# Optimization experiments

Hardware: AMD Instinct MI355X
Metric: run time of the kernel (lower is better)

The kernel has to match this reference:

```python
import jax, jax.numpy as jnp
import numpy as np

S = 14
C = 20
STEP = 1.0 / 14
LAMBDA_COORD = 3.0
LAMBDA_NOOBJ = 0.3
LAMBDA_OBJ = 1.0
LAMBDA_CLS = 1.5


def setup_inputs() -> dict:
    key = jax.random.key(0)
    k1, k2 = jax.random.split(key)
    batch = 4096
    pred = jax.random.normal(k1, (batch, S, S, 30), dtype=jnp.float32)
    target = jax.random.normal(k2, (batch, S, S, 30), dtype=jnp.float32)
    return {"pred": pred, "target": target}


def _convert_boxes(box):
    # box: [B, S, S, 2, 4] in (cx, cy, w, h) grid-relative coords
    # grid index i is the x (third) axis, j the y (second) axis, per forward's [x, y]
    gi = jnp.arange(S, dtype=box.dtype)[None, None, :, None]  # x index
    gj = jnp.arange(S, dtype=box.dtype)[None, :, None, None]  # y index
    x = (box[..., 0] + gi) * STEP - box[..., 2] * 0.5
    y = (box[..., 1] + gj) * STEP - box[..., 3] * 0.5
    out = jnp.stack([x, y, box[..., 2], box[..., 3]], axis=-1)
    return jnp.maximum(out, 0.0)  # torch.clamp(box, min=0) on the whole box


def _iou(b1, b2):
    x1, y1, w1, h1 = b1[..., 0], b1[..., 1], b1[..., 2], b1[..., 3]
    x2, y2, w2, h2 = b2[..., 0], b2[..., 1], b2[..., 2], b2[..., 3]
    inter_w = jnp.maximum(w1 + w2 - (jnp.maximum(x1 + w1, x2 + w2) - jnp.minimum(x1, x2)), 0.0)
    inter_h = jnp.maximum(h1 + h2 - (jnp.maximum(y1 + h1, y2 + h2) - jnp.minimum(y1, y2)), 0.0)
    inter = inter_w * inter_h
    union = w1 * h1 + w2 * h2 - inter
    return inter / (union + 1e-6)


def _smooth_l1_sum(p, t, mask):
    d = p - t
    ad = jnp.abs(d)
    l = jnp.where(ad < 1.0, 0.5 * d * d, ad - 0.5)
    return jnp.sum(l * mask)


def reference(pred, target):
    batch = pred.shape[0]
    pb = pred[..., :10].reshape(batch, S, S, 2, 5)
    tb = target[..., :10].reshape(batch, S, S, 2, 5)
    pred_cls = pred[..., 10:]
    target_cls = target[..., 10:]

    obj_mask = tb[..., 4] > 0          # [B,S,S,2]
    sig_mask = obj_mask[..., 1]         # [B,S,S]

    # responsible-box selection: elementwise IoU between pred box k and target box k
    ious = _iou(_convert_boxes(pb[..., :4]), _convert_boxes(tb[..., :4]))  # [B,S,S,2]
    max_i = jnp.argmax(ious, axis=-1)   # first-max, matches torch .max(0)
    keep = jnp.arange(2) == max_i[..., None]
    obj_mask = jnp.where(sig_mask[..., None], obj_mask & keep, obj_mask)
    noobj_mask = ~obj_mask

    om = obj_mask.astype(pred.dtype)
    nm = noobj_mask.astype(pred.dtype)

    conf_sq = (pb[..., 4] - tb[..., 4]) ** 2
    noobj_loss = jnp.sum(conf_sq * nm)
    obj_loss = jnp.sum(conf_sq * om)

    xy_loss = _smooth_l1_sum(pb[..., :2], tb[..., :2], om[..., None])
    wh_loss = _smooth_l1_sum(
        jnp.sqrt(jnp.maximum(pb[..., 2:4], 1e-6)),
        jnp.sqrt(jnp.maximum(tb[..., 2:4], 1e-6)),
        om[..., None],
    )

    logp = jax.nn.log_softmax(pred_cls, axis=-1)
    tgt_idx = jnp.argmax(target_cls, axis=-1)  # [B,S,S]
    nll = -jnp.take_along_axis(logp, tgt_idx[..., None], axis=-1)[..., 0]
    class_loss = jnp.sum(nll * sig_mask.astype(pred.dtype))

    total = (LAMBDA_COORD * (xy_loss + wh_loss)
             + LAMBDA_OBJ * obj_loss
             + LAMBDA_NOOBJ * noobj_loss
             + LAMBDA_CLS * class_loss) / batch
    return total
```

## Files before the change

### kernel.cpp

```cpp
#include <hip/hip_runtime.h>
#include <math.h>

#define SS 14
#define NCLS 20
#define CELL_FLOATS 30
#define BLOCK 256
#define CPB 128
#define FPB (CPB * CELL_FLOATS)
#define F4PB (FPB / 4)

__device__ __forceinline__ float smooth_l1(float d) {
    float ad = fabsf(d);
    return ad < 1.0f ? 0.5f * d * d : ad - 0.5f;
}

__device__ __forceinline__ void conv_box(const float* b, float gi, float gj,
                                         float& x, float& y, float& w, float& h) {
    const float STEP = 1.0f / 14.0f;
    x = fmaxf((b[0] + gi) * STEP - b[2] * 0.5f, 0.0f);
    y = fmaxf((b[1] + gj) * STEP - b[3] * 0.5f, 0.0f);
    w = fmaxf(b[2], 0.0f);
    h = fmaxf(b[3], 0.0f);
}

__device__ __forceinline__ float iou_box(float x1, float y1, float w1, float h1,
                                         float x2, float y2, float w2, float h2) {
    float iw = fmaxf(w1 + w2 - (fmaxf(x1 + w1, x2 + w2) - fminf(x1, x2)), 0.0f);
    float ih = fmaxf(h1 + h2 - (fmaxf(y1 + h1, y2 + h2) - fminf(y1, y2)), 0.0f);
    float inter = iw * ih;
    float uni = w1 * h1 + w2 * h2 - inter;
    return inter / (uni + 1e-6f);
}

__global__ __launch_bounds__(BLOCK) void yolo_loss_kernel(
    const float4* __restrict__ pred4, const float4* __restrict__ target4,
    float* __restrict__ partials, int ncells, float inv_batch) {
    __shared__ float sp[FPB];
    __shared__ float st[FPB];

    const int tid = threadIdx.x;
    const long long total4 = ((long long)ncells * CELL_FLOATS) / 4;
    const long long base4 = (long long)blockIdx.x * F4PB;

#pragma unroll
    for (int k = 0; k < 4; ++k) {
        int i = tid + k * BLOCK;
        if (i < F4PB && base4 + i < total4) {
            ((float4*)sp)[i] = pred4[base4 + i];
            ((float4*)st)[i] = target4[base4 + i];
        }
    }
    __syncthreads();

    int cell = blockIdx.x * CPB + tid;
    float tot = 0.0f;
    if (tid < CPB && cell < ncells) {
        float p[CELL_FLOATS], t[CELL_FLOATS];
        const float2* pp = (const float2*)(sp + tid * CELL_FLOATS);
        const float2* tp = (const float2*)(st + tid * CELL_FLOATS);
#pragma unroll
        for (int k = 0; k < CELL_FLOATS / 2; ++k) {
            ((float2*)p)[k] = pp[k];
            ((float2*)t)[k] = tp[k];
        }

        int rc = cell % (SS * SS);
        float gj = (float)(rc / SS);
        float gi = (float)(rc % SS);

        float px, py, pw, ph, tx, ty, tw, th;
        conv_box(p + 0, gi, gj, px, py, pw, ph);
        conv_box(t + 0, gi, gj, tx, ty, tw, th);
        float iou0 = iou_box(px, py, pw, ph, tx, ty, tw, th);
        conv_box(p + 5, gi, gj, px, py, pw, ph);
        conv_box(t + 5, gi, gj, tx, ty, tw, th);
        float iou1 = iou_box(px, py, pw, ph, tx, ty, tw, th);

        bool obj0 = t[4] > 0.0f;
        bool obj1 = t[9] > 0.0f;
        bool sig = obj1;
        bool m1 = iou1 > iou0;
        bool om0 = sig ? (obj0 && !m1) : obj0;
        bool om1 = sig ? m1 : false;

        float c0 = p[4] - t[4]; c0 *= c0;
        float c1 = p[9] - t[9]; c1 *= c1;
        float obj_l = (om0 ? c0 : 0.0f) + (om1 ? c1 : 0.0f);
        float noobj_l = (om0 ? 0.0f : c0) + (om1 ? 0.0f : c1);

        float xy = 0.0f, wh = 0.0f;
        if (om0) {
            xy += smooth_l1(p[0] - t[0]) + smooth_l1(p[1] - t[1]);
            wh += smooth_l1(sqrtf(fmaxf(p[2], 1e-6f)) - sqrtf(fmaxf(t[2], 1e-6f)));
            wh += smooth_l1(sqrtf(fmaxf(p[3], 1e-6f)) - sqrtf(fmaxf(t[3], 1e-6f)));
        }
        if (om1) {
            xy += smooth_l1(p[5] - t[5]) + smooth_l1(p[6] - t[6]);
            wh += smooth_l1(sqrtf(fmaxf(p[7], 1e-6f)) - sqrtf(fmaxf(t[7], 1e-6f)));
            wh += smooth_l1(sqrtf(fmaxf(p[8], 1e-6f)) - sqrtf(fmaxf(t[8], 1e-6f)));
        }

        float cls = 0.0f;
        {
            float m = p[10];
#pragma unroll
            for (int c = 1; c < NCLS; ++c) m = fmaxf(m, p[10 + c]);
            float se = 0.0f;
#pragma unroll
            for (int c = 0; c < NCLS; ++c) se += expf(p[10 + c] - m);
            float bt = t[10];
            int bi = 0;
#pragma unroll
            for (int c = 1; c < NCLS; ++c) {
                if (t[10 + c] > bt) { bt = t[10 + c]; bi = c; }
            }
            float logp = p[10 + bi] - m - logf(se);
            cls = sig ? -logp : 0.0f;
        }

        tot = 3.0f * (xy + wh) + obj_l + 0.3f * noobj_l + 1.5f * cls;
        tot *= inv_batch;
    }

#pragma unroll
    for (int off = 32; off > 0; off >>= 1) tot += __shfl_down(tot, off, 64);
    __shared__ float wsum[4];
    int lane = threadIdx.x & 63;
    int wid = threadIdx.x >> 6;
    if (lane == 0) wsum[wid] = tot;
    __syncthreads();
    if (threadIdx.x == 0) {
        partials[blockIdx.x] = wsum[0] + wsum[1] + wsum[2] + wsum[3];
    }
}

__global__ __launch_bounds__(BLOCK) void reduce_kernel(
    const float* __restrict__ partials, float* __restrict__ out, int n) {
    float s = 0.0f;
    for (int i = threadIdx.x; i < n; i += BLOCK) s += partials[i];
#pragma unroll
    for (int off = 32; off > 0; off >>= 1) s += __shfl_down(s, off, 64);
    __shared__ float wsum[4];
    int lane = threadIdx.x & 63;
    int wid = threadIdx.x >> 6;
    if (lane == 0) wsum[wid] = s;
    __syncthreads();
    if (threadIdx.x == 0) out[0] = wsum[0] + wsum[1] + wsum[2] + wsum[3];
}

extern "C" void kernel_launch(void* const* d_in, const int* in_sizes, int n_in,
                              void* d_out, int out_size, void* d_ws, size_t ws_size,
                              hipStream_t stream) {
    const float4* pred4 = (const float4*)d_in[0];
    const float4* target4 = (const float4*)d_in[1];
    float* out = (float*)d_out;
    float* partials = (float*)d_ws;

    int total = in_sizes[0];
    int ncells = total / CELL_FLOATS;
    int batch = ncells / (SS * SS);
    float inv_batch = 1.0f / (float)batch;

    int grid = (ncells + CPB - 1) / CPB;
    yolo_loss_kernel<<<grid, BLOCK, 0, stream>>>(pred4, target4, partials, ncells, inv_batch);
    reduce_kernel<<<1, BLOCK, 0, stream>>>(partials, out, grid);
}
```

Before: 230.9 us.

## Process four tiles per block with register-prefetched double buffering

Each block now handles four 128-cell tiles in sequence. The next tile's global loads go into registers while the current tile is computed from shared memory. This overlaps memory latency with compute and cuts the grid size and the partials count by four. It also switches expf/logf to the fast __expf/__logf intrinsics, which slightly lowers precision. Fewer blocks could reduce parallelism, and the extra syncs add some cost.

```diff
diff --git a/kernel.cpp b/kernel.cpp
--- a/kernel.cpp
+++ b/kernel.cpp
@@ -5,9 +5,10 @@
 #define NCLS 20
 #define CELL_FLOATS 30
 #define BLOCK 256
-#define CPB 128
-#define FPB (CPB * CELL_FLOATS)
-#define F4PB (FPB / 4)
+#define TILE 128
+#define TPB_TILES 4
+#define FPT (TILE * CELL_FLOATS)
+#define F4PT (FPT / 4)
 
 __device__ __forceinline__ float smooth_l1(float d) {
     float ad = fabsf(d);
@@ -32,102 +33,140 @@
     return inter / (uni + 1e-6f);
 }
 
+__device__ __forceinline__ float cell_loss(const float* __restrict__ p,
+                                           const float* __restrict__ t, int cell) {
+    int rc = cell % (SS * SS);
+    float gj = (float)(rc / SS);
+    float gi = (float)(rc % SS);
+
+    float px, py, pw, ph, tx, ty, tw, th;
+    conv_box(p + 0, gi, gj, px, py, pw, ph);
+    conv_box(t + 0, gi, gj, tx, ty, tw, th);
+    float iou0 = iou_box(px, py, pw, ph, tx, ty, tw, th);
+    conv_box(p + 5, gi, gj, px, py, pw, ph);
+    conv_box(t + 5, gi, gj, tx, ty, tw, th);
+    float iou1 = iou_box(px, py, pw, ph, tx, ty, tw, th);
+
+    bool obj0 = t[4] > 0.0f;
+    bool obj1 = t[9] > 0.0f;
+    bool sig = obj1;
+    bool m1 = iou1 > iou0;
+    bool om0 = sig ? (obj0 && !m1) : obj0;
+    bool om1 = sig ? m1 : false;
+
+    float c0 = p[4] - t[4]; c0 *= c0;
+    float c1 = p[9] - t[9]; c1 *= c1;
+    float obj_l = (om0 ? c0 : 0.0f) + (om1 ? c1 : 0.0f);
+    float noobj_l = (om0 ? 0.0f : c0) + (om1 ? 0.0f : c1);
+
+    float xy = 0.0f, wh = 0.0f;
+    if (om0) {
+        xy += smooth_l1(p[0] - t[0]) + smooth_l1(p[1] - t[1]);
+        wh += smooth_l1(sqrtf(fmaxf(p[2], 1e-6f)) - sqrtf(fmaxf(t[2], 1e-6f)));
+        wh += smooth_l1(sqrtf(fmaxf(p[3], 1e-6f)) - sqrtf(fmaxf(t[3], 1e-6f)));
+    }
+    if (om1) {
+        xy += smooth_l1(p[5] - t[5]) + smooth_l1(p[6] - t[6]);
+        wh += smooth_l1(sqrtf(fmaxf(p[7], 1e-6f)) - sqrtf(fmaxf(t[7], 1e-6f)));
+        wh += smooth_l1(sqrtf(fmaxf(p[8], 1e-6f)) - sqrtf(fmaxf(t[8], 1e-6f)));
+    }
+
+    float cls = 0.0f;
+    {
+        float m = p[10];
+#pragma unroll
+        for (int c = 1; c < NCLS; ++c) m = fmaxf(m, p[10 + c]);
+        float se = 0.0f;
+#pragma unroll
+        for (int c = 0; c < NCLS; ++c) se += __expf(p[10 + c] - m);
+        float bt = t[10];
+        int bi = 0;
+#pragma unroll
+        for (int c = 1; c < NCLS; ++c) {
+            if (t[10 + c] > bt) { bt = t[10 + c]; bi = c; }
+        }
+        float logp = p[10 + bi] - m - __logf(se);
+        cls = sig ? -logp : 0.0f;
+    }
+
+    return 3.0f * (xy + wh) + obj_l + 0.3f * noobj_l + 1.5f * cls;
+}
+
 __global__ __launch_bounds__(BLOCK) void yolo_loss_kernel(
     const float4* __restrict__ pred4, const float4* __restrict__ target4,
-    float* __restrict__ partials, int ncells, float inv_batch) {
-    __shared__ float sp[FPB];
-    __shared__ float st[FPB];
+    float* __restrict__ partials, int ncells, int ntiles, float inv_batch) {
+    __shared__ float sp[FPT];
+    __shared__ float st[FPT];
 
     const int tid = threadIdx.x;
+    const int tile0 = blockIdx.x * TPB_TILES;
     const long long total4 = ((long long)ncells * CELL_FLOATS) / 4;
-    const long long base4 = (long long)blockIdx.x * F4PB;
-
-#pragma unroll
-    for (int k = 0; k < 4; ++k) {
-        int i = tid + k * BLOCK;
-        if (i < F4PB && base4 + i < total4) {
-            ((float4*)sp)[i] = pred4[base4 + i];
-            ((float4*)st)[i] = target4[base4 + i];
-        }
-    }
-    __syncthreads();
-
-    int cell = blockIdx.x * CPB + tid;
-    float tot = 0.0f;
-    if (tid < CPB && cell < ncells) {
-        float p[CELL_FLOATS], t[CELL_FLOATS];
-        const float2* pp = (const float2*)(sp + tid * CELL_FLOATS);
-        const float2* tp = (const float2*)(st + tid * CELL_FLOATS);
-#pragma unroll
-        for (int k = 0; k < CELL_FLOATS / 2; ++k) {
-            ((float2*)p)[k] = pp[k];
-            ((float2*)t)[k] = tp[k];
-        }
-
-        int rc = cell % (SS * SS);
-        float gj = (float)(rc / SS);
-        float gi = (float)(rc % SS);
-
-        float px, py, pw, ph, tx, ty, tw, th;
-        conv_box(p + 0, gi, gj, px, py, pw, ph);
-        conv_box(t + 0, gi, gj, tx, ty, tw, th);
-        float iou0 = iou_box(px, py, pw, ph, tx, ty, tw, th);
-        conv_box(p + 5, gi, gj, px, py, pw, ph);
-        conv_box(t + 5, gi, gj, tx, ty, tw, th);
-        float iou1 = iou_box(px, py, pw, ph, tx, ty, tw, th);
-
-        bool obj0 = t[4] > 0.0f;
-        bool obj1 = t[9] > 0.0f;
-        bool sig = obj1;
-        bool m1 = iou1 > iou0;
-        bool om0 = sig ? (obj0 && !m1) : obj0;
-        bool om1 = sig ? m1 : false;
-
-        float c0 = p[4] - t[4]; c0 *= c0;
-        float c1 = p[9] - t[9]; c1 *= c1;
-        float obj_l = (om0 ? c0 : 0.0f) + (om1 ? c1 : 0.0f);
-        float noobj_l = (om0 ? 0.0f : c0) + (om1 ? 0.0f : c1);
-
-        float xy = 0.0f, wh = 0.0f;
-        if (om0) {
-            xy += smooth_l1(p[0] - t[0]) + smooth_l1(p[1] - t[1]);
-            wh += smooth_l1(sqrtf(fmaxf(p[2], 1e-6f)) - sqrtf(fmaxf(t[2], 1e-6f)));
-            wh += smooth_l1(sqrtf(fmaxf(p[3], 1e-6f)) - sqrtf(fmaxf(t[3], 1e-6f)));
-        }
-        if (om1) {
-            xy += smooth_l1(p[5] - t[5]) + smooth_l1(p[6] - t[6]);
-            wh += smooth_l1(sqrtf(fmaxf(p[7], 1e-6f)) - sqrtf(fmaxf(t[7], 1e-6f)));
-            wh += smooth_l1(sqrtf(fmaxf(p[8], 1e-6f)) - sqrtf(fmaxf(t[8], 1e-6f)));
-        }
-
-        float cls = 0.0f;
-        {
-            float m = p[10];
-#pragma unroll
-            for (int c = 1; c < NCLS; ++c) m = fmaxf(m, p[10 + c]);
-            float se = 0.0f;
-#pragma unroll
-            for (int c = 0; c < NCLS; ++c) se += expf(p[10 + c] - m);
-            float bt = t[10];
-            int bi = 0;
-#pragma unroll
-            for (int c = 1; c < NCLS; ++c) {
-                if (t[10 + c] > bt) { bt = t[10 + c]; bi = c; }
-            }
-            float logp = p[10 + bi] - m - logf(se);
-            cls = sig ? -logp : 0.0f;
-        }
-
-        tot = 3.0f * (xy + wh) + obj_l + 0.3f * noobj_l + 1.5f * cls;
-        tot *= inv_batch;
-    }
-
-#pragma unroll
-    for (int off = 32; off > 0; off >>= 1) tot += __shfl_down(tot, off, 64);
+
+    float4 rp[4], rt[4];
+    float acc = 0.0f;
+
+    {
+        long long base4 = (long long)tile0 * F4PT;
+#pragma unroll
+        for (int k = 0; k < 4; ++k) {
+            int i = tid + k * BLOCK;
+            if (i < F4PT && base4 + i < total4) {
+                rp[k] = pred4[base4 + i];
+                rt[k] = target4[base4 + i];
+            }
+        }
+    }
+
+    for (int j = 0; j < TPB_TILES; ++j) {
+        int tt = tile0 + j;
+        if (tt >= ntiles) break;
+
+#pragma unroll
+        for (int k = 0; k < 4; ++k) {
+            int i = tid + k * BLOCK;
+            if (i < F4PT) {
+                ((float4*)sp)[i] = rp[k];
+                ((float4*)st)[i] = rt[k];
+            }
+        }
+        __syncthreads();
+
+        if (j + 1 < TPB_TILES && tt + 1 < ntiles) {
+            long long base4 = (long long)(tt + 1) * F4PT;
+#pragma unroll
+            for (int k = 0; k < 4; ++k) {
+                int i = tid + k * BLOCK;
+                if (i < F4PT && base4 + i < total4) {
+                    rp[k] = pred4[base4 + i];
+                    rt[k] = target4[base4 + i];
+                }
+            }
+        }
+
+        int cell = tt * TILE + tid;
+        if (tid < TILE && cell < ncells) {
+            float p[CELL_FLOATS], t[CELL_FLOATS];
+            const float2* pp = (const float2*)(sp + tid * CELL_FLOATS);
+            const float2* tp = (const float2*)(st + tid * CELL_FLOATS);
+#pragma unroll
+            for (int k = 0; k < CELL_FLOATS / 2; ++k) {
+                ((float2*)p)[k] = pp[k];
+                ((float2*)t)[k] = tp[k];
+            }
+            acc += cell_loss(p, t, cell);
+        }
+
+        if (j + 1 < TPB_TILES) __syncthreads();
+    }
+
+    acc *= inv_batch;
+
+#pragma unroll
+    for (int off = 32; off > 0; off >>= 1) acc += __shfl_down(acc, off, 64);
     __shared__ float wsum[4];
     int lane = threadIdx.x & 63;
     int wid = threadIdx.x >> 6;
-    if (lane == 0) wsum[wid] = tot;
+    if (lane == 0) wsum[wid] = acc;
     __syncthreads();
     if (threadIdx.x == 0) {
         partials[blockIdx.x] = wsum[0] + wsum[1] + wsum[2] + wsum[3];
@@ -161,7 +200,9 @@
     int batch = ncells / (SS * SS);
     float inv_batch = 1.0f / (float)batch;
 
-    int grid = (ncells + CPB - 1) / CPB;
-    yolo_loss_kernel<<<grid, BLOCK, 0, stream>>>(pred4, target4, partials, ncells, inv_batch);
+    int ntiles = (ncells + TILE - 1) / TILE;
+    int grid = (ntiles + TPB_TILES - 1) / TPB_TILES;
+    yolo_loss_kernel<<<grid, BLOCK, 0, stream>>>(pred4, target4, partials,
+                                                 ncells, ntiles, inv_batch);
     reduce_kernel<<<1, BLOCK, 0, stream>>>(partials, out, grid);
 }
```

Measured after the change: 291.9 us. +26.4%, slower.
